# Optimization experiments

Measured on AMD Instinct MI355X. Metric: run time of the kernel, lower is better.

## Reference

```python
import jax, jax.numpy as jnp
import numpy as np

B, S, D = 4, 2048, 1024
H = 16
HD = D // H  # head_dim = 64


def setup_inputs() -> dict:
    key = jax.random.key(0)
    ks = jax.random.split(key, 5)
    scale = 1.0 / np.sqrt(D)
    return {
        "x": jax.random.normal(ks[0], (B, S, D), dtype=jnp.float32),
        "Wq": jax.random.normal(ks[1], (D, D), dtype=jnp.float32) * scale,
        "Wk": jax.random.normal(ks[2], (D, D), dtype=jnp.float32) * scale,
        "Wv": jax.random.normal(ks[3], (D, D), dtype=jnp.float32) * scale,
        "Wo": jax.random.normal(ks[4], (D, D), dtype=jnp.float32) * scale,
        "bo": jnp.zeros((D,), dtype=jnp.float32),
    }


def reference(x, Wq, Wk, Wv, Wo, bo):
    b, s, d = x.shape
    # project and split heads: [b, h, s, hd]
    q = (x @ Wq).reshape(b, s, H, HD).transpose(0, 2, 1, 3)
    k = (x @ Wk).reshape(b, s, H, HD).transpose(0, 2, 1, 3)
    v = (x @ Wv).reshape(b, s, H, HD).transpose(0, 2, 1, 3)
    # scores: [b, h, s, s]
    scores = jnp.einsum("bhqd,bhkd->bhqk", q, k)
    # NOTE: original uses tril(diagonal=1) -> allows one future token (off-by-one)
    mask = jnp.tril(jnp.ones((s, s), dtype=bool), k=1)
    scores = jnp.where(mask, scores, -jnp.inf)
    attn = jax.nn.softmax(scores / np.sqrt(HD), axis=-1)
    # dropout p=0.0 (deterministic baseline): identity
    ctx = jnp.einsum("bhqk,bhkd->bhqd", attn, v)
    ctx = ctx.transpose(0, 2, 1, 3).reshape(b, s, d)
    return ctx @ Wo + bo
```

## Files before the change

### kernel.cpp

```cpp
#include <hip/hip_runtime.h>
#include <hip/hip_bf16.h>

#define Bq 4
#define Sq 2048
#define Dq 1024
#define Hq 16
#define HDq 64
#define Mq (Bq*Sq)

typedef unsigned short u16;
typedef __attribute__((ext_vector_type(8))) __bf16 b16x8;
typedef __attribute__((ext_vector_type(4))) float f32x4;
typedef __attribute__((ext_vector_type(4))) unsigned int u32x4;

__device__ inline float bf2f(u16 h){ union{unsigned u; float f;} v; v.u = ((unsigned)h)<<16; return v.f; }
__device__ inline u16 f2bf(float f){ union{float f; unsigned u;} v; v.f=f; unsigned r = v.u + 0x7FFFu + ((v.u>>16)&1u); return (u16)(r>>16); }
__device__ inline u16 truncbf(float f){ union{float f; unsigned u;} v; v.f=f; return (u16)(v.u>>16); }
__device__ inline float ld_elem(const void* p, size_t i, int isf32){
  return isf32 ? ((const float*)p)[i] : bf2f(((const u16*)p)[i]);
}
__device__ inline void ld16(const u16* g, u16* l){
  __builtin_amdgcn_global_load_lds((const __attribute__((address_space(1))) void*)g,
                                   (__attribute__((address_space(3))) void*)l, 16, 0, 0);
}

#if __has_builtin(__builtin_amdgcn_exp2f)
#define EXP2(x) __builtin_amdgcn_exp2f(x)
#else
#define EXP2(x) __expf((x)*0.69314718056f)
#endif
#define SCALE_LOG2E 0.18033688011112042f

__global__ void detect_dtype(const unsigned* __restrict__ x, int* __restrict__ flag){
  __shared__ int cnt;
  if(threadIdx.x==0) cnt=0;
  __syncthreads();
  int local=0;
  for(int i=threadIdx.x;i<2048;i+=256){
    unsigned w = x[i];
    if(((w>>7)&0xFFu)>=0x90u) local++;
    if(((w>>23)&0xFFu)>=0x90u) local++;
  }
  atomicAdd(&cnt, local);
  __syncthreads();
  if(threadIdx.x==0) *flag = (cnt>64) ? 1 : 0;
}

__global__ __launch_bounds__(256) void convert_x(const void* __restrict__ x, u16* __restrict__ xc,
                                                 const int* __restrict__ flag, int n){
  const int f = *flag;
  int i = (blockIdx.x*256 + threadIdx.x)*8;
  if(i>=n) return;
  if(f){
    const float* xf=(const float*)x;
    #pragma unroll
    for(int j=0;j<8;j++) xc[i+j] = f2bf(xf[i+j]);
  } else {
    *(u32x4*)&xc[i] = *(const u32x4*)((const u16*)x + i);
  }
}

__global__ __launch_bounds__(256) void transpose_w(
    const void* __restrict__ W0, const void* __restrict__ W1,
    const void* __restrict__ W2, const void* __restrict__ W3,
    u16* __restrict__ T0, u16* __restrict__ T1,
    u16* __restrict__ T2, u16* __restrict__ T3,
    const int* __restrict__ flag){
  __shared__ u16 tile[64][65];
  const int f = *flag;
  const int z = blockIdx.z;
  const void* src = (z==0)?W0:(z==1)?W1:(z==2)?W2:W3;
  u16*       dst = (z==0)?T0:(z==1)?T1:(z==2)?T2:T3;
  const int t = threadIdx.x;
  const int k0 = blockIdx.x*64, n0 = blockIdx.y*64;
  #pragma unroll
  for(int r=0;r<16;r++){
    int row = r*4 + (t>>6), col = t&63;
    tile[row][col] = f2bf(ld_elem(src, (size_t)(k0+row)*Dq + n0 + col, f));
  }
  __syncthreads();
  #pragma unroll
  for(int r=0;r<16;r++){
    int row = r*4 + (t>>6), col = t&63;
    dst[(size_t)(n0+row)*Dq + k0 + col] = tile[col][row];
  }
}

template<int MODE>
__global__ __launch_bounds__(256, 2) void gemm2p(
    const u16* __restrict__ A, const u16* __restrict__ Bt,
    u16* __restrict__ O0, u16* __restrict__ O1, u16* __restrict__ O2,
    void* __restrict__ Og, const void* __restrict__ bias, const int* __restrict__ flag){
  constexpr int BM = (MODE==0)?256:128;
  constexpr int MF = (MODE==0)?8:4;
  constexpr int NT = Dq/32;
  __shared__ u16 Asl[3][BM*32];
  __shared__ u16 Bsl[3][128*32];
  const int f = (MODE==1) ? *flag : 0;
  const int t = threadIdx.x;
  const int lane = t & 63, wave = t >> 6;
  const int quad = lane >> 4, l16 = lane & 15;
  const int wr = wave >> 1, wc = wave & 1;
  int L = blockIdx.x + blockIdx.y*gridDim.x;
  int k8 = L & 7, ii = L >> 3;
  int m0, n0;
  if (MODE==0){
    int nsb = ii >> 5, rem = ii & 31;
    int mg = rem >> 3, ng = rem & 7;
    m0 = (k8*4 + mg)*256; n0 = (nsb*8 + ng)*128;
  } else {
    int mg = ii >> 3, ng = ii & 7;
    m0 = (k8*8 + mg)*128; n0 = ng*128;
  }

  f32x4 acc[MF][4] = {};

  auto stageA = [&](int T, int s){
    #pragma unroll
    for(int r=0;r<BM/64;r++){
      int idx = t + (r<<8);
      int row = idx>>2, g = idx&3;
      int gl = g ^ ((row>>1)&3);
      ld16(&A[(size_t)(m0+row)*Dq + (T<<5) + gl*8], &Asl[s][idx*8]);
    }
  };
  auto stageB = [&](int T, int s){
    #pragma unroll
    for(int r=0;r<2;r++){
      int idx = t + (r<<8);
      int row = idx>>2, g = idx&3;
      int gl = g ^ ((row>>1)&3);
      ld16(&Bt[(size_t)(n0+row)*Dq + (T<<5) + gl*8], &Bsl[s][idx*8]);
    }
  };
  auto ldA = [&](int s, int i)->b16x8{
    int row = wr*(MF*16) + i*16 + l16;
    return *(const b16x8*)&Asl[s][row*32 + ((quad ^ ((row>>1)&3))<<3)];
  };
  auto ldB = [&](int s, int j)->b16x8{
    int row = wc*64 + j*16 + l16;
    return *(const b16x8*)&Bsl[s][row*32 + ((quad ^ ((row>>1)&3))<<3)];
  };
  #define MFMA_BF16 __builtin_amdgcn_mfma_f32_16x16x32_bf16

  stageA(0,0); stageB(0,0); stageA(1,1); stageB(1,1);
  if (MODE==0) asm volatile("s_waitcnt vmcnt(6)" ::: "memory");
  else         asm volatile("s_waitcnt vmcnt(4)" ::: "memory");
  __builtin_amdgcn_s_barrier();
  __builtin_amdgcn_sched_barrier(0);

  int s0=0, s1=1, s2=2;
  for(int tt=0; tt<NT; ++tt){
    if (MODE==0){
      if(tt+2<NT) stageA(tt+2, s2);
      b16x8 af[4], bf[4];
      #pragma unroll
      for(int i=0;i<4;i++) af[i]=ldA(s0,i);
      #pragma unroll
      for(int j=0;j<4;j++) bf[j]=ldB(s0,j);
      __builtin_amdgcn_s_barrier();
      asm volatile("s_waitcnt lgkmcnt(0)" ::: "memory");
      __builtin_amdgcn_sched_barrier(0);
      __builtin_amdgcn_s_setprio(1);
      #pragma unroll
      for(int i=0;i<4;i++)
        #pragma unroll
        for(int j=0;j<4;j++)
          acc[i][j]=MFMA_BF16(af[i],bf[j],acc[i][j],0,0,0);
      __builtin_amdgcn_s_setprio(0);
      __builtin_amdgcn_s_barrier();
      __builtin_amdgcn_sched_barrier(0);
      if(tt+2<NT) stageB(tt+2, s2);
      #pragma unroll
      for(int i=0;i<4;i++) af[i]=ldA(s0,4+i);
      __builtin_amdgcn_s_barrier();
      asm volatile("s_waitcnt lgkmcnt(0)" ::: "memory");
      __builtin_amdgcn_sched_barrier(0);
      __builtin_amdgcn_s_setprio(1);
      #pragma unroll
      for(int i=0;i<4;i++)
        #pragma unroll
        for(int j=0;j<4;j++)
          acc[4+i][j]=MFMA_BF16(af[i],bf[j],acc[4+i][j],0,0,0);
      __builtin_amdgcn_s_setprio(0);
      if(tt<NT-2) asm volatile("s_waitcnt vmcnt(6)" ::: "memory");
      else        asm volatile("s_waitcnt vmcnt(0)" ::: "memory");
      __builtin_amdgcn_s_barrier();
      __builtin_amdgcn_sched_barrier(0);
    } else {
      if(tt+2<NT){ stageA(tt+2, s2); stageB(tt+2, s2); }
      b16x8 af[4], bf[4];
      #pragma unroll
      for(int i=0;i<4;i++) af[i]=ldA(s0,i);
      #pragma unroll
      for(int j=0;j<4;j++) bf[j]=ldB(s0,j);
      __builtin_amdgcn_s_barrier();
      asm volatile("s_waitcnt lgkmcnt(0)" ::: "memory");
      __builtin_amdgcn_sched_barrier(0);
      __builtin_amdgcn_s_setprio(1);
      #pragma unroll
      for(int i=0;i<4;i++)
        #pragma unroll
        for(int j=0;j<4;j++)
          acc[i][j]=MFMA_BF16(af[i],bf[j],acc[i][j],0,0,0);
      __builtin_amdgcn_s_setprio(0);
      if(tt<NT-2) asm volatile("s_waitcnt vmcnt(4)" ::: "memory");
      else        asm volatile("s_waitcnt vmcnt(0)" ::: "memory");
      __builtin_amdgcn_s_barrier();
      __builtin_amdgcn_sched_barrier(0);
    }
    int x=s0; s0=s1; s1=s2; s2=x;
  }

  #pragma unroll
  for(int i=0;i<MF;i++){
    #pragma unroll
    for(int j=0;j<4;j++){
      int n = n0 + wc*64 + j*16 + l16;
      #pragma unroll
      for(int r=0;r<4;r++){
        int m = m0 + wr*(MF*16) + i*16 + quad*4 + r;
        float c = acc[i][j][r];
        if (MODE==1){
          float c2 = c + ld_elem(bias, n, f);
          if (f) ((float*)Og)[(size_t)m*Dq + n] = c2;
          else   ((u16*)Og)[(size_t)m*Dq + n]   = f2bf(c2);
        } else {
          int z = n >> 10, nn2 = n & 1023;
          int b = m >> 11, s = m & 2047;
          int h = nn2 >> 6, hd = nn2 & 63;
          if (z==0)      O0[(((size_t)(b*Hq + h))*Sq + s)*HDq + hd] = f2bf(c*SCALE_LOG2E);
          else if (z==1) O1[(((size_t)(b*Hq + h))*Sq + s)*HDq + hd] = f2bf(c);
          else           O2[(((size_t)(b*Hq + h))*HDq + hd)*Sq + s] = f2bf(c);
        }
      }
    }
  }
  #undef MFMA_BF16
}

__global__ __launch_bounds__(256) void flash_attn(
    const u16* __restrict__ Q, const u16* __restrict__ K,
    const u16* __restrict__ VT, u16* __restrict__ C){
  __shared__ u16 Kt[128*64];
  __shared__ u16 Vt[64*128];
  __shared__ u16 Pl[4][16][72];
  const int t = threadIdx.x;
  const int lane = t&63, wave = t>>6, quad = lane>>4, l16 = lane&15;
  int L  = blockIdx.x + blockIdx.y*gridDim.x;
  int k8 = L & 7, ii = L >> 3;
  const int bh = k8*8 + (ii>>4);
  const int p  = ii & 15;
  const int b = bh >> 4, h = bh & 15;
  const int qt[2] = { p, 31 - p };
  int nk[2];
  #pragma unroll
  for(int tt=0;tt<2;tt++){ int v = qt[tt]+2; nk[tt] = (v<32)?v:32; }
  const int nrounds = (nk[1]+1)>>1;
  const u16* Qh = Q  + (size_t)bh*Sq*HDq;
  const u16* Kh = K  + (size_t)bh*Sq*HDq;
  const u16* Vh = VT + (size_t)bh*HDq*Sq;

  b16x8 aq[2][2];
  #pragma unroll
  for(int tt=0;tt<2;tt++){
    const u16* qp = Qh + (size_t)(qt[tt]*64 + wave*16 + l16)*HDq + quad*8;
    aq[tt][0] = *(const b16x8*)qp;
    aq[tt][1] = *(const b16x8*)(qp + 32);
  }
  b16x8 vone;
  #pragma unroll
  for(int i=0;i<8;i++) vone[i] = (__bf16)1.0f;

  const f32x4 fzero = {0.f,0.f,0.f,0.f};
  f32x4 Oa[2][4]; f32x4 lacc[2];
  #pragma unroll
  for(int tt=0;tt<2;tt++){ lacc[tt]=fzero; for(int j=0;j<4;j++) Oa[tt][j]=fzero; }

  for(int kt2=0; kt2<nrounds; kt2++){
    __syncthreads();
    #pragma unroll
    for(int r=0;r<4;r++){
      int idx = t + (r<<8);
      int row = idx>>3, g = idx&7;
      int csw = (g ^ (row&7))<<3;
      ld16(Kh + (size_t)(kt2*128+row)*HDq + csw, Kt + idx*8);
    }
    #pragma unroll
    for(int r=0;r<4;r++){
      int idx = t + (r<<8);
      int row = idx>>4, g = idx&15;
      int csw = (g ^ (row&15))<<3;
      ld16(Vh + (size_t)row*Sq + (size_t)kt2*128 + csw, Vt + idx*8);
    }
    __syncthreads();

    #pragma unroll
    for(int half=0; half<2; half++){
      const int kt = kt2*2 + half;
      #pragma unroll
      for(int tt=0;tt<2;tt++){
        if (kt >= nk[tt]) continue;
        const int qq0 = qt[tt]*64;
        f32x4 sc[4];
        #pragma unroll
        for(int jn=0;jn<4;jn++){
          int krow = half*64 + jn*16 + l16;
          const u16* kp = &Kt[krow*64];
          f32x4 s = fzero;
          b16x8 bk0 = *(const b16x8*)&kp[((quad     ^ (krow&7))<<3)];
          b16x8 bk1 = *(const b16x8*)&kp[(((quad+4) ^ (krow&7))<<3)];
          s = __builtin_amdgcn_mfma_f32_16x16x32_bf16(aq[tt][0], bk0, s, 0,0,0);
          s = __builtin_amdgcn_mfma_f32_16x16x32_bf16(aq[tt][1], bk1, s, 0,0,0);
          sc[jn] = s;
        }
        if (kt < qt[tt]) {
          #pragma unroll
          for(int jn=0;jn<4;jn++)
            #pragma unroll
            for(int r=0;r<4;r++)
              Pl[wave][quad*4+r][jn*16+l16] = truncbf(EXP2(sc[jn][r]));
        } else {
          const int qbase = qq0 + wave*16 + quad*4;
          #pragma unroll
          for(int jn=0;jn<4;jn++){
            int kg = kt*64 + jn*16 + l16;
            #pragma unroll
            for(int r=0;r<4;r++){
              float sv = sc[jn][r];
              if (kg > qbase + r + 1) sv = -__builtin_inff();
              Pl[wave][quad*4+r][jn*16+l16] = truncbf(EXP2(sv));
            }
          }
        }
        #pragma unroll
        for(int ks=0;ks<2;ks++){
          b16x8 ap = *(const b16x8*)&Pl[wave][l16][ks*32 + quad*8];
          int glog = half*8 + ks*4 + quad;
          #pragma unroll
          for(int jd=0;jd<4;jd++){
            int hd = jd*16 + l16;
            b16x8 bv = *(const b16x8*)&Vt[hd*128 + ((glog ^ (hd&15))<<3)];
            Oa[tt][jd] = __builtin_amdgcn_mfma_f32_16x16x32_bf16(ap, bv, Oa[tt][jd], 0,0,0);
          }
          lacc[tt] = __builtin_amdgcn_mfma_f32_16x16x32_bf16(ap, vone, lacc[tt], 0,0,0);
        }
      }
    }
  }
  #pragma unroll
  for(int tt=0;tt<2;tt++){
    const int qq0 = qt[tt]*64;
    #pragma unroll
    for(int r=0;r<4;r++){
      int s = qq0 + wave*16 + quad*4 + r;
      float inv = 1.0f / lacc[tt][r];
      #pragma unroll
      for(int jd=0;jd<4;jd++)
        C[((size_t)(b*Sq + s))*Dq + h*HDq + jd*16 + l16] = f2bf(Oa[tt][jd][r]*inv);
    }
  }
}

extern "C" void kernel_launch(void* const* d_in, const int* in_sizes, int n_in,
                              void* d_out, int out_size, void* d_ws, size_t ws_size,
                              hipStream_t stream){
  const void* x  = d_in[0];
  const void* Wq = d_in[1];
  const void* Wk = d_in[2];
  const void* Wv = d_in[3];
  const void* Wo = d_in[4];
  const void* bo = d_in[5];

  char* ws = (char*)d_ws;
  size_t off = 0;
  auto wsalloc = [&](size_t bytes)->void*{
    void* p = ws + off; off += (bytes + 255) & ~(size_t)255; return p;
  };
  int* flag = (int*)wsalloc(256);
  u16* WqT = (u16*)wsalloc((size_t)Dq*Dq*2);
  u16* WkT = (u16*)wsalloc((size_t)Dq*Dq*2);
  u16* WvT = (u16*)wsalloc((size_t)Dq*Dq*2);
  u16* WoT = (u16*)wsalloc((size_t)Dq*Dq*2);
  u16* xc  = (u16*)wsalloc((size_t)Mq*Dq*2);
  u16* Qb  = (u16*)wsalloc((size_t)Mq*Dq*2);
  u16* Kb  = (u16*)wsalloc((size_t)Mq*Dq*2);
  u16* VTb = (u16*)wsalloc((size_t)Mq*Dq*2);
  u16* Cb  = (u16*)wsalloc((size_t)Mq*Dq*2);

  detect_dtype<<<1, 256, 0, stream>>>((const unsigned*)x, flag);
  convert_x<<<dim3(Mq*Dq/8/256), 256, 0, stream>>>(x, xc, flag, Mq*Dq);
  transpose_w<<<dim3(16,16,4), 256, 0, stream>>>(Wq,Wk,Wv,Wo, WqT,WkT,WvT,WoT, flag);
  gemm2p<0><<<dim3(24, 32), 256, 0, stream>>>(xc, WqT, Qb,Kb,VTb, nullptr, nullptr, flag);
  flash_attn<<<dim3(16, Bq*Hq), 256, 0, stream>>>(Qb, Kb, VTb, Cb);
  gemm2p<1><<<dim3(8, 64), 256, 0, stream>>>(Cb, WoT, nullptr,nullptr,nullptr, d_out, bo, flag);
}
```

Measured before the change: 208.3 us.

## Use 8-wave 256x256 tiles for fused QKV projection GEMM

Replaces the templated QKV projection GEMM (256x128 tiles, 4 waves) with a dedicated 512-thread kernel computing 256x256 output tiles, halving grid size and raising arithmetic intensity per staged byte. The output projection GEMM is split into its own non-templated kernel with unchanged logic. The larger tile doubles B-tile LDS use to 96KB per block, which may limit occupancy to one block per CU despite the launch bound of 2.

```diff
diff --git a/kernel.cpp b/kernel.cpp
--- a/kernel.cpp
+++ b/kernel.cpp
@@ -86,38 +86,138 @@
   }
 }
 
-template<int MODE>
-__global__ __launch_bounds__(256, 2) void gemm2p(
+__global__ __launch_bounds__(512, 2) void gemm8w(
     const u16* __restrict__ A, const u16* __restrict__ Bt,
-    u16* __restrict__ O0, u16* __restrict__ O1, u16* __restrict__ O2,
+    u16* __restrict__ O0, u16* __restrict__ O1, u16* __restrict__ O2){
+  constexpr int NT = Dq/32;
+  __shared__ u16 Asl[3][256*32];
+  __shared__ u16 Bsl[3][256*32];
+  const int t = threadIdx.x;
+  const int lane = t & 63, wave = t >> 6;
+  const int quad = lane >> 4, l16 = lane & 15;
+  const int wr = wave >> 2, wc = wave & 3;
+  int L = blockIdx.x + blockIdx.y*gridDim.x;
+  int k8 = L & 7, ii = L >> 3;
+  int mg = ii & 3, ng = ii >> 2;
+  const int m0 = (k8*4 + mg)*256, n0 = ng*256;
+
+  f32x4 acc[8][4] = {};
+
+  auto stageA = [&](int T, int s){
+    #pragma unroll
+    for(int r=0;r<2;r++){
+      int idx = t + (r<<9);
+      int row = idx>>2, g = idx&3;
+      int gl = g ^ ((row>>1)&3);
+      ld16(&A[(size_t)(m0+row)*Dq + (T<<5) + gl*8], &Asl[s][idx*8]);
+    }
+  };
+  auto stageB = [&](int T, int s){
+    #pragma unroll
+    for(int r=0;r<2;r++){
+      int idx = t + (r<<9);
+      int row = idx>>2, g = idx&3;
+      int gl = g ^ ((row>>1)&3);
+      ld16(&Bt[(size_t)(n0+row)*Dq + (T<<5) + gl*8], &Bsl[s][idx*8]);
+    }
+  };
+  auto ldA = [&](int s, int i)->b16x8{
+    int row = wr*128 + i*16 + l16;
+    return *(const b16x8*)&Asl[s][row*32 + ((quad ^ ((row>>1)&3))<<3)];
+  };
+  auto ldB = [&](int s, int j)->b16x8{
+    int row = wc*64 + j*16 + l16;
+    return *(const b16x8*)&Bsl[s][row*32 + ((quad ^ ((row>>1)&3))<<3)];
+  };
+  #define MFMA_BF16 __builtin_amdgcn_mfma_f32_16x16x32_bf16
+
+  stageA(0,0); stageB(0,0); stageA(1,1); stageB(1,1);
+  asm volatile("s_waitcnt vmcnt(4)" ::: "memory");
+  __builtin_amdgcn_s_barrier();
+  __builtin_amdgcn_sched_barrier(0);
+
+  int s0=0, s1=1, s2=2;
+  for(int tt=0; tt<NT; ++tt){
+    b16x8 a[8], b[4];
+    #pragma unroll
+    for(int i=0;i<4;i++) a[i]=ldA(s0,i);
+    #pragma unroll
+    for(int j=0;j<4;j++) b[j]=ldB(s0,j);
+    if(tt+2<NT) stageA(tt+2, s2);
+    __builtin_amdgcn_s_barrier();
+    asm volatile("s_waitcnt lgkmcnt(0)" ::: "memory");
+    __builtin_amdgcn_sched_barrier(0);
+    __builtin_amdgcn_s_setprio(1);
+    #pragma unroll
+    for(int i=0;i<4;i++)
+      #pragma unroll
+      for(int j=0;j<4;j++)
+        acc[i][j]=MFMA_BF16(a[i],b[j],acc[i][j],0,0,0);
+    __builtin_amdgcn_s_setprio(0);
+    __builtin_amdgcn_s_barrier();
+    __builtin_amdgcn_sched_barrier(0);
+    #pragma unroll
+    for(int i=0;i<4;i++) a[4+i]=ldA(s0,4+i);
+    if(tt+2<NT) stageB(tt+2, s2);
+    __builtin_amdgcn_s_barrier();
+    asm volatile("s_waitcnt lgkmcnt(0)" ::: "memory");
+    __builtin_amdgcn_sched_barrier(0);
+    __builtin_amdgcn_s_setprio(1);
+    #pragma unroll
+    for(int i=0;i<4;i++)
+      #pragma unroll
+      for(int j=0;j<4;j++)
+        acc[4+i][j]=MFMA_BF16(a[4+i],b[j],acc[4+i][j],0,0,0);
+    __builtin_amdgcn_s_setprio(0);
+    if(tt<NT-2)       asm volatile("s_waitcnt vmcnt(4)" ::: "memory");
+    else if(tt==NT-2) asm volatile("s_waitcnt vmcnt(0)" ::: "memory");
+    __builtin_amdgcn_s_barrier();
+    __builtin_amdgcn_sched_barrier(0);
+    int x=s0; s0=s1; s1=s2; s2=x;
+  }
+
+  #pragma unroll
+  for(int i=0;i<8;i++){
+    #pragma unroll
+    for(int j=0;j<4;j++){
+      int n = n0 + wc*64 + j*16 + l16;
+      #pragma unroll
+      for(int r=0;r<4;r++){
+        int m = m0 + wr*128 + i*16 + quad*4 + r;
+        float c = acc[i][j][r];
+        int z = n >> 10, nn2 = n & 1023;
+        int b2 = m >> 11, s = m & 2047;
+        int h = nn2 >> 6, hd = nn2 & 63;
+        if (z==0)      O0[(((size_t)(b2*Hq + h))*Sq + s)*HDq + hd] = f2bf(c*SCALE_LOG2E);
+        else if (z==1) O1[(((size_t)(b2*Hq + h))*Sq + s)*HDq + hd] = f2bf(c);
+        else           O2[(((size_t)(b2*Hq + h))*HDq + hd)*Sq + s] = f2bf(c);
+      }
+    }
+  }
+  #undef MFMA_BF16
+}
+
+__global__ __launch_bounds__(256, 2) void gemm_op(
+    const u16* __restrict__ A, const u16* __restrict__ Bt,
     void* __restrict__ Og, const void* __restrict__ bias, const int* __restrict__ flag){
-  constexpr int BM = (MODE==0)?256:128;
-  constexpr int MF = (MODE==0)?8:4;
   constexpr int NT = Dq/32;
-  __shared__ u16 Asl[3][BM*32];
+  __shared__ u16 Asl[3][128*32];
   __shared__ u16 Bsl[3][128*32];
-  const int f = (MODE==1) ? *flag : 0;
+  const int f = *flag;
   const int t = threadIdx.x;
   const int lane = t & 63, wave = t >> 6;
   const int quad = lane >> 4, l16 = lane & 15;
   const int wr = wave >> 1, wc = wave & 1;
   int L = blockIdx.x + blockIdx.y*gridDim.x;
   int k8 = L & 7, ii = L >> 3;
-  int m0, n0;
-  if (MODE==0){
-    int nsb = ii >> 5, rem = ii & 31;
-    int mg = rem >> 3, ng = rem & 7;
-    m0 = (k8*4 + mg)*256; n0 = (nsb*8 + ng)*128;
-  } else {
-    int mg = ii >> 3, ng = ii & 7;
-    m0 = (k8*8 + mg)*128; n0 = ng*128;
-  }
-
-  f32x4 acc[MF][4] = {};
+  int mg = ii >> 3, ng = ii & 7;
+  const int m0 = (k8*8 + mg)*128, n0 = ng*128;
+
+  f32x4 acc[4][4] = {};
 
   auto stageA = [&](int T, int s){
     #pragma unroll
-    for(int r=0;r<BM/64;r++){
+    for(int r=0;r<2;r++){
       int idx = t + (r<<8);
       int row = idx>>2, g = idx&3;
       int gl = g ^ ((row>>1)&3);
@@ -134,7 +234,7 @@
     }
   };
   auto ldA = [&](int s, int i)->b16x8{
-    int row = wr*(MF*16) + i*16 + l16;
+    int row = wr*64 + i*16 + l16;
     return *(const b16x8*)&Asl[s][row*32 + ((quad ^ ((row>>1)&3))<<3)];
   };
   auto ldB = [&](int s, int j)->b16x8{
@@ -144,95 +244,46 @@
   #define MFMA_BF16 __builtin_amdgcn_mfma_f32_16x16x32_bf16
 
   stageA(0,0); stageB(0,0); stageA(1,1); stageB(1,1);
-  if (MODE==0) asm volatile("s_waitcnt vmcnt(6)" ::: "memory");
-  else         asm volatile("s_waitcnt vmcnt(4)" ::: "memory");
+  asm volatile("s_waitcnt vmcnt(4)" ::: "memory");
   __builtin_amdgcn_s_barrier();
   __builtin_amdgcn_sched_barrier(0);
 
   int s0=0, s1=1, s2=2;
   for(int tt=0; tt<NT; ++tt){
-    if (MODE==0){
-      if(tt+2<NT) stageA(tt+2, s2);
-      b16x8 af[4], bf[4];
-      #pragma unroll
-      for(int i=0;i<4;i++) af[i]=ldA(s0,i);
-      #pragma unroll
-      for(int j=0;j<4;j++) bf[j]=ldB(s0,j);
-      __builtin_amdgcn_s_barrier();
-      asm volatile("s_waitcnt lgkmcnt(0)" ::: "memory");
-      __builtin_amdgcn_sched_barrier(0);
-      __builtin_amdgcn_s_setprio(1);
-      #pragma unroll
-      for(int i=0;i<4;i++)
-        #pragma unroll
-        for(int j=0;j<4;j++)
-          acc[i][j]=MFMA_BF16(af[i],bf[j],acc[i][j],0,0,0);
-      __builtin_amdgcn_s_setprio(0);
-      __builtin_amdgcn_s_barrier();
-      __builtin_amdgcn_sched_barrier(0);
-      if(tt+2<NT) stageB(tt+2, s2);
-      #pragma unroll
-      for(int i=0;i<4;i++) af[i]=ldA(s0,4+i);
-      __builtin_amdgcn_s_barrier();
-      asm volatile("s_waitcnt lgkmcnt(0)" ::: "memory");
-      __builtin_amdgcn_sched_barrier(0);
-      __builtin_amdgcn_s_setprio(1);
-      #pragma unroll
-      for(int i=0;i<4;i++)
-        #pragma unroll
-        for(int j=0;j<4;j++)
-          acc[4+i][j]=MFMA_BF16(af[i],bf[j],acc[4+i][j],0,0,0);
-      __builtin_amdgcn_s_setprio(0);
-      if(tt<NT-2) asm volatile("s_waitcnt vmcnt(6)" ::: "memory");
-      else        asm volatile("s_waitcnt vmcnt(0)" ::: "memory");
-      __builtin_amdgcn_s_barrier();
-      __builtin_amdgcn_sched_barrier(0);
-    } else {
-      if(tt+2<NT){ stageA(tt+2, s2); stageB(tt+2, s2); }
-      b16x8 af[4], bf[4];
-      #pragma unroll
-      for(int i=0;i<4;i++) af[i]=ldA(s0,i);
-      #pragma unroll
-      for(int j=0;j<4;j++) bf[j]=ldB(s0,j);
-      __builtin_amdgcn_s_barrier();
-      asm volatile("s_waitcnt lgkmcnt(0)" ::: "memory");
-      __builtin_amdgcn_sched_barrier(0);
-      __builtin_amdgcn_s_setprio(1);
-      #pragma unroll
-      for(int i=0;i<4;i++)
-        #pragma unroll
-        for(int j=0;j<4;j++)
-          acc[i][j]=MFMA_BF16(af[i],bf[j],acc[i][j],0,0,0);
-      __builtin_amdgcn_s_setprio(0);
-      if(tt<NT-2) asm volatile("s_waitcnt vmcnt(4)" ::: "memory");
-      else        asm volatile("s_waitcnt vmcnt(0)" ::: "memory");
-      __builtin_amdgcn_s_barrier();
-      __builtin_amdgcn_sched_barrier(0);
-    }
+    if(tt+2<NT){ stageA(tt+2, s2); stageB(tt+2, s2); }
+    b16x8 af[4], bf[4];
+    #pragma unroll
+    for(int i=0;i<4;i++) af[i]=ldA(s0,i);
+    #pragma unroll
+    for(int j=0;j<4;j++) bf[j]=ldB(s0,j);
+    __builtin_amdgcn_s_barrier();
+    asm volatile("s_waitcnt lgkmcnt(0)" ::: "memory");
+    __builtin_amdgcn_sched_barrier(0);
+    __builtin_amdgcn_s_setprio(1);
+    #pragma unroll
+    for(int i=0;i<4;i++)
+      #pragma unroll
+      for(int j=0;j<4;j++)
+        acc[i][j]=MFMA_BF16(af[i],bf[j],acc[i][j],0,0,0);
+    __builtin_amdgcn_s_setprio(0);
+    if(tt<NT-2) asm volatile("s_waitcnt vmcnt(4)" ::: "memory");
+    else        asm volatile("s_waitcnt vmcnt(0)" ::: "memory");
+    __builtin_amdgcn_s_barrier();
+    __builtin_amdgcn_sched_barrier(0);
     int x=s0; s0=s1; s1=s2; s2=x;
   }
 
   #pragma unroll
-  for(int i=0;i<MF;i++){
+  for(int i=0;i<4;i++){
     #pragma unroll
     for(int j=0;j<4;j++){
       int n = n0 + wc*64 + j*16 + l16;
       #pragma unroll
       for(int r=0;r<4;r++){
-        int m = m0 + wr*(MF*16) + i*16 + quad*4 + r;
-        float c = acc[i][j][r];
-        if (MODE==1){
-          float c2 = c + ld_elem(bias, n, f);
-          if (f) ((float*)Og)[(size_t)m*Dq + n] = c2;
-          else   ((u16*)Og)[(size_t)m*Dq + n]   = f2bf(c2);
-        } else {
-          int z = n >> 10, nn2 = n & 1023;
-          int b = m >> 11, s = m & 2047;
-          int h = nn2 >> 6, hd = nn2 & 63;
-          if (z==0)      O0[(((size_t)(b*Hq + h))*Sq + s)*HDq + hd] = f2bf(c*SCALE_LOG2E);
-          else if (z==1) O1[(((size_t)(b*Hq + h))*Sq + s)*HDq + hd] = f2bf(c);
-          else           O2[(((size_t)(b*Hq + h))*HDq + hd)*Sq + s] = f2bf(c);
-        }
+        int m = m0 + wr*64 + i*16 + quad*4 + r;
+        float c2 = acc[i][j][r] + ld_elem(bias, n, f);
+        if (f) ((float*)Og)[(size_t)m*Dq + n] = c2;
+        else   ((u16*)Og)[(size_t)m*Dq + n]   = f2bf(c2);
       }
     }
   }
@@ -391,7 +442,7 @@
   detect_dtype<<<1, 256, 0, stream>>>((const unsigned*)x, flag);
   convert_x<<<dim3(Mq*Dq/8/256), 256, 0, stream>>>(x, xc, flag, Mq*Dq);
   transpose_w<<<dim3(16,16,4), 256, 0, stream>>>(Wq,Wk,Wv,Wo, WqT,WkT,WvT,WoT, flag);
-  gemm2p<0><<<dim3(24, 32), 256, 0, stream>>>(xc, WqT, Qb,Kb,VTb, nullptr, nullptr, flag);
+  gemm8w<<<dim3(12, 32), 512, 0, stream>>>(xc, WqT, Qb,Kb,VTb);
   flash_attn<<<dim3(16, Bq*Hq), 256, 0, stream>>>(Qb, Kb, VTb, Cb);
-  gemm2p<1><<<dim3(8, 64), 256, 0, stream>>>(Cb, WoT, nullptr,nullptr,nullptr, d_out, bo, flag);
-}
+  gemm_op<<<dim3(8, 64), 256, 0, stream>>>(Cb, WoT, d_out, bo, flag);
+}
```

Result: slower. 222.4 us (+6.8%).
